# Optimization experiments

Hardware: AMD Instinct MI355X
Metric: run time of the kernel (lower is better)

## Reference

```python
import jax, jax.numpy as jnp
import numpy as np

EMBED = 384
HEADS = 12
DH = EMBED // HEADS  # 32, lucidrains default dim_heads = dim // heads
EPS = 1e-5


def _layernorm(t, g, b):
    mu = jnp.mean(t, axis=-1, keepdims=True)
    var = jnp.mean(jnp.square(t - mu), axis=-1, keepdims=True)
    return (t - mu) * jax.lax.rsqrt(var + EPS) * g + b


def _self_attn(t2, Wq, Wkv, Wo, bo):
    # t2: (N, T, D) -> multi-head self attention (lucidrains SelfAttention)
    N, T, D = t2.shape
    q = t2 @ Wq
    k, v = jnp.split(t2 @ Wkv, 2, axis=-1)
    def split_heads(z):
        return z.reshape(N, T, HEADS, DH).transpose(0, 2, 1, 3)  # (N,H,T,DH)
    q, k, v = map(split_heads, (q, k, v))
    dots = jnp.einsum('nhie,nhje->nhij', q, k) * (DH ** -0.5)
    o = jnp.einsum('nhij,nhje->nhie', jax.nn.softmax(dots, axis=-1), v)
    o = o.transpose(0, 2, 1, 3).reshape(N, T, D)
    return o @ Wo + bo


def _axial(xcl, axis, Wq, Wkv, Wo, bo):
    # xcl channels-last: (b, 3, 16, 16, C); attend along `axis` (1, 2 or 3)
    y = jnp.moveaxis(xcl, axis, -2)
    sh = y.shape
    o = _self_attn(y.reshape(-1, sh[-2], sh[-1]), Wq, Wkv, Wo, bo)
    return jnp.moveaxis(o.reshape(sh), -2, axis)


def setup_inputs() -> dict:
    key = jax.random.key(0)
    ks = jax.random.split(key, 24)
    d, mlp = EMBED, 4 * EMBED
    s = 0.02
    inp = {'x': jax.random.normal(ks[0], (128, 384, 3, 16, 16), jnp.float32)}
    for i in range(3):  # one SelfAttention per axial dim (slice, h, w)
        inp[f'Wq{i}'] = (jax.random.normal(ks[1 + 3 * i], (d, d)) * s).astype(jnp.float32)
        inp[f'Wkv{i}'] = (jax.random.normal(ks[2 + 3 * i], (d, 2 * d)) * s).astype(jnp.float32)
        inp[f'Wo{i}'] = (jax.random.normal(ks[3 + 3 * i], (d, d)) * s).astype(jnp.float32)
        inp[f'bo{i}'] = jnp.zeros((d,), jnp.float32)
    inp['g1'] = jnp.ones((d,), jnp.float32)
    inp['be1'] = jnp.zeros((d,), jnp.float32)
    inp['W1m'] = (jax.random.normal(ks[10], (d, mlp)) * s).astype(jnp.float32)
    inp['b1m'] = jnp.zeros((mlp,), jnp.float32)
    inp['W2m'] = (jax.random.normal(ks[11], (mlp, d)) * s).astype(jnp.float32)
    inp['b2m'] = jnp.zeros((d,), jnp.float32)
    inp['g2'] = jnp.ones((d,), jnp.float32)
    inp['be2'] = jnp.zeros((d,), jnp.float32)
    return inp


def reference(x, Wq0, Wkv0, Wo0, bo0, Wq1, Wkv1, Wo1, bo1, Wq2, Wkv2, Wo2, bo2,
              g1, be1, W1m, b1m, W2m, b2m, g2, be2):
    # x: (B, C=384, 3, 16, 16); dropout is identity in eval mode
    xcl = jnp.moveaxis(x, 1, -1)  # (B, 3, 16, 16, C)
    attn = (_axial(xcl, 1, Wq0, Wkv0, Wo0, bo0)
            + _axial(xcl, 2, Wq1, Wkv1, Wo1, bo1)
            + _axial(xcl, 3, Wq2, Wkv2, Wo2, bo2))  # sum_axial_out=True
    xcl = xcl + attn  # residual
    B = xcl.shape[0]
    t = xcl.reshape(B, 3 * 16 * 16, EMBED)  # == x.flatten(2).transpose(1,2)
    t = _layernorm(t, g1, be1)
    m = jax.nn.gelu(t @ W1m + b1m, approximate=False) @ W2m + b2m
    t = _layernorm(t + m, g2, be2)
    return jnp.moveaxis(t.reshape(B, 3, 16, 16, EMBED), -1, 1)
```

## Files before the change

kernel.cpp:

```cpp
#include <hip/hip_runtime.h>

typedef unsigned short u16;
typedef __bf16 bf16;
typedef bf16  bf16x4 __attribute__((ext_vector_type(4)));
typedef bf16  bf16x8 __attribute__((ext_vector_type(8)));
typedef float f32x4  __attribute__((ext_vector_type(4)));

__device__ __forceinline__ u16  f2b(float v) { return __builtin_bit_cast(u16, (bf16)v); }
__device__ __forceinline__ float b2f(u16 b)  { return (float)__builtin_bit_cast(bf16, b); }

__global__ void probe_dtype(const float* xf, int* flag) {
    __shared__ int cnt[256];
    const int tid = threadIdx.x;
    int good = 0;
#pragma unroll
    for (int i = 0; i < 4; ++i) {
        const float a = fabsf(xf[tid * 4 + i]);
        if (a > 9.5e-7f && a < 1.0e6f) good++;
    }
    cnt[tid] = good;
    __syncthreads();
    if (tid == 0) { int s = 0; for (int i = 0; i < 256; ++i) s += cnt[i]; *flag = (s > 512) ? 1 : 0; }
}

__global__ void cvt_vec(const void* in, bf16* out, int n, const int* flag) {
    const int f32 = *flag;
    for (int i = blockIdx.x * 256 + threadIdx.x; i < n; i += gridDim.x * 256)
        out[i] = f32 ? (bf16)(((const float*)in)[i])
                     : __builtin_bit_cast(bf16, ((const u16*)in)[i]);
}

__global__ void sum3_vec(const void* a, const void* b, const void* c, bf16* out, int n, const int* flag) {
    const int f32 = *flag;
    for (int i = blockIdx.x * 256 + threadIdx.x; i < n; i += gridDim.x * 256) {
        float va, vb, vc;
        if (f32) { va = ((const float*)a)[i]; vb = ((const float*)b)[i]; vc = ((const float*)c)[i]; }
        else { va = b2f(((const u16*)a)[i]); vb = b2f(((const u16*)b)[i]); vc = b2f(((const u16*)c)[i]); }
        out[i] = (bf16)(va + vb + vc);
    }
}

__global__ void transpose_cvt(const void* in, u16* out, size_t base_off, int R, int C, int ostride, const int* flag) {
    __shared__ u16 tile[32][34];
    const int f32 = *flag;
    const int c0 = blockIdx.x * 32, r0 = blockIdx.y * 32;
    const size_t bi = base_off + (size_t)blockIdx.z * R * C;
    const size_t bo = (size_t)blockIdx.z * C * ostride;
    const int tx = threadIdx.x, ty = threadIdx.y;
#pragma unroll
    for (int i = 0; i < 4; ++i) {
        const size_t idx = bi + (size_t)(r0 + ty + i * 8) * C + c0 + tx;
        tile[ty + i * 8][tx] = f32 ? f2b(((const float*)in)[idx]) : ((const u16*)in)[idx];
    }
    __syncthreads();
#pragma unroll
    for (int i = 0; i < 4; ++i)
        out[bo + (size_t)(c0 + ty + i * 8) * ostride + r0 + tx] = tile[tx][ty + i * 8];
}

__global__ void transpose_out(const u16* in, void* out, size_t base_off, int R, int C, const int* flag) {
    __shared__ u16 tile[32][34];
    const int f32 = *flag;
    const int c0 = blockIdx.x * 32, r0 = blockIdx.y * 32;
    const size_t bi = (size_t)blockIdx.z * R * C;
    const size_t bo = base_off + (size_t)blockIdx.z * R * C;
    const int tx = threadIdx.x, ty = threadIdx.y;
#pragma unroll
    for (int i = 0; i < 4; ++i)
        tile[ty + i * 8][tx] = in[bi + (size_t)(r0 + ty + i * 8) * C + c0 + tx];
    __syncthreads();
#pragma unroll
    for (int i = 0; i < 4; ++i) {
        const size_t o = bo + (size_t)(c0 + ty + i * 8) * R + r0 + tx;
        const u16 v = tile[tx][ty + i * 8];
        if (f32) ((float*)out)[o] = b2f(v); else ((u16*)out)[o] = v;
    }
}

__device__ __forceinline__ void gld_lds16(const bf16* g, bf16* l) {
    __builtin_amdgcn_global_load_lds((__attribute__((address_space(1))) void*)g,
                                     (__attribute__((address_space(3))) void*)l,
                                     16, 0, 0);
}

template<int MODE>
__global__ __launch_bounds__(512)
void gemm256(const bf16* __restrict__ A, const bf16* __restrict__ BT,
             bf16* C, const bf16* __restrict__ bias, int M, int N, int K)
{
    __shared__ __align__(16) bf16 sm[65536];
    const int tid = threadIdx.x;

    const int gx = gridDim.x, gy = gridDim.y;
    int lin = blockIdx.y * gx + blockIdx.x;
    const int nwg = gx * gy;
    const int q = nwg >> 3, r8 = nwg & 7;
    const int xcd = lin & 7, idx = lin >> 3;
    lin = (xcd < r8 ? xcd * (q + 1) : r8 * (q + 1) + (xcd - r8) * q) + idx;
    const int bm0 = (lin / gy) * 256;
    const int bn0 = (lin % gy) * 256;

    const int lane = tid & 63, wid = tid >> 6;
    const int wr = wid >> 2, wc = wid & 3;
    const int fr = lane & 15, fg = lane >> 4;
    const int arow = tid >> 3;
    const int scol = ((tid & 7) ^ (arow & 7)) << 3;

    const bf16* Ab = A  + (size_t)(bm0 + arow) * K + scol;
    const bf16* Bb = BT + (size_t)(bn0 + arow) * K + scol;

    bf16* const lA0 = sm;
    bf16* const lA1 = sm + 16384;
    bf16* const lB0 = sm + 32768;
    bf16* const lB1 = sm + 49152;

    f32x4 acc[8][4] = {};
    const int NT = K >> 6;

#pragma unroll
    for (int i = 0; i < 4; ++i) gld_lds16(Ab + (size_t)i * 64 * K, lA0 + i * 4096 + tid * 8);
#pragma unroll
    for (int i = 0; i < 4; ++i) gld_lds16(Bb + (size_t)i * 64 * K, lB0 + i * 4096 + tid * 8);
    __syncthreads();

    const int sw = fr & 7;
    for (int t = 0; t < NT; ++t) {
        if (t + 1 < NT) {
            const int k0 = (t + 1) << 6;
            bf16* la = ((t + 1) & 1) ? lA1 : lA0;
            bf16* lb = ((t + 1) & 1) ? lB1 : lB0;
#pragma unroll
            for (int i = 0; i < 4; ++i) gld_lds16(Ab + k0 + (size_t)i * 64 * K, la + i * 4096 + tid * 8);
#pragma unroll
            for (int i = 0; i < 4; ++i) gld_lds16(Bb + k0 + (size_t)i * 64 * K, lb + i * 4096 + tid * 8);
        }
        const bf16* la = (t & 1) ? lA1 : lA0;
        const bf16* lb = (t & 1) ? lB1 : lB0;
#pragma unroll
        for (int kk = 0; kk < 2; ++kk) {
            const int so = ((((kk << 2) + fg) ^ sw) << 3);
            bf16x8 bfv[4];
#pragma unroll
            for (int n = 0; n < 4; ++n)
                bfv[n] = *(const bf16x8*)&lb[(wc * 64 + n * 16 + fr) * 64 + so];
#pragma unroll
            for (int m = 0; m < 8; ++m) {
                const bf16x8 af = *(const bf16x8*)&la[(wr * 128 + m * 16 + fr) * 64 + so];
#pragma unroll
                for (int n = 0; n < 4; ++n)
                    acc[m][n] = __builtin_amdgcn_mfma_f32_16x16x32_bf16(af, bfv[n], acc[m][n], 0, 0, 0);
            }
        }
        __syncthreads();
    }

#pragma unroll
    for (int n = 0; n < 4; ++n) {
        const int col = wc * 64 + n * 16 + fr;
        const float bv = (MODE == 2) ? (float)bias[bn0 + col] : 0.f;
#pragma unroll
        for (int m = 0; m < 8; ++m) {
            const int row0 = wr * 128 + m * 16 + fg * 4;
#pragma unroll
            for (int r = 0; r < 4; ++r) {
                float v = acc[m][n][r];
                if (MODE == 2) { v += bv; v = 0.5f * v * (1.f + erff(v * 0.70710678118654752f)); }
                sm[(row0 + r) * 256 + col] = (bf16)v;
            }
        }
    }
    __syncthreads();
#pragma unroll
    for (int it = 0; it < 16; ++it) {
        const int chunk = it * 512 + tid;
        const int row = chunk >> 5, c8 = (chunk & 31) << 3;
        *(bf16x8*)&C[(size_t)(bm0 + row) * N + bn0 + c8] = *(const bf16x8*)&sm[row * 256 + c8];
    }
}

template<int MODE>
__global__ __launch_bounds__(256)
void gemm_bt(const bf16* __restrict__ A, const bf16* __restrict__ BT,
             bf16* C, const bf16* __restrict__ bias,
             const bf16* add, int M, int N, int K)
{
    __shared__ __align__(16) bf16 sm[16384];
    const int tid = threadIdx.x;

    const int gx = gridDim.x, gy = gridDim.y;
    int lin = blockIdx.y * gx + blockIdx.x;
    const int nwg = gx * gy;
    const int q = nwg >> 3, r8 = nwg & 7;
    const int xcd = lin & 7, idx = lin >> 3;
    lin = (xcd < r8 ? xcd * (q + 1) : r8 * (q + 1) + (xcd - r8) * q) + idx;
    const int bm0 = (lin / gy) * 128;
    const int bn0 = (lin % gy) * 128;

    const int lane = tid & 63, wid = tid >> 6;
    const int wr = wid >> 1, wc = wid & 1;
    const int fr = lane & 15, fg = lane >> 4;
    const int arow = tid >> 3;
    const int scol = ((tid & 7) ^ (arow & 7)) << 3;

    const bf16* Ab = A  + (size_t)(bm0 + arow) * K + scol;
    const bf16* Bb = BT + (size_t)(bn0 + arow) * K + scol;

    bf16* const lA = sm;
    bf16* const lB = sm + 8192;

    f32x4 acc[4][4] = {};
    const int NT = K >> 6;
    const int sw = fr & 7;

    for (int t = 0; t < NT; ++t) {
        __syncthreads();
        const int k0 = t << 6;
#pragma unroll
        for (int i = 0; i < 4; ++i) gld_lds16(Ab + k0 + (size_t)i * 32 * K, lA + i * 2048 + tid * 8);
#pragma unroll
        for (int i = 0; i < 4; ++i) gld_lds16(Bb + k0 + (size_t)i * 32 * K, lB + i * 2048 + tid * 8);
        __syncthreads();
#pragma unroll
        for (int kk = 0; kk < 2; ++kk) {
            bf16x8 af[4], bfv[4];
#pragma unroll
            for (int m = 0; m < 4; ++m)
                af[m] = *(const bf16x8*)&lA[(wr * 64 + m * 16 + fr) * 64 + ((((kk << 2) + fg) ^ sw) << 3)];
#pragma unroll
            for (int n = 0; n < 4; ++n)
                bfv[n] = *(const bf16x8*)&lB[(wc * 64 + n * 16 + fr) * 64 + ((((kk << 2) + fg) ^ sw) << 3)];
#pragma unroll
            for (int m = 0; m < 4; ++m)
#pragma unroll
                for (int n = 0; n < 4; ++n)
                    acc[m][n] = __builtin_amdgcn_mfma_f32_16x16x32_bf16(af[m], bfv[n], acc[m][n], 0, 0, 0);
        }
    }
    __syncthreads();

    float* lc = (float*)sm;
#pragma unroll
    for (int half = 0; half < 2; ++half) {
        if (wr == half) {
#pragma unroll
            for (int n = 0; n < 4; ++n) {
                const int col = wc * 64 + n * 16 + fr;
#pragma unroll
                for (int m = 0; m < 4; ++m)
#pragma unroll
                    for (int r2 = 0; r2 < 4; ++r2)
                        lc[(m * 16 + fg * 4 + r2) * 128 + col] = acc[m][n][r2];
            }
        }
        __syncthreads();
#pragma unroll
        for (int i = 0; i < 8; ++i) {
            const int chunk = i * 256 + tid;
            const int row = chunk >> 5, cb = (chunk & 31) * 4;
            const size_t goff = (size_t)(bm0 + half * 64 + row) * N + bn0 + cb;
            const f32x4 v = ((const f32x4*)lc)[chunk];
            bf16x4 o;
            if (MODE == 1) {
                const bf16x4 bv = *(const bf16x4*)&bias[bn0 + cb];
                const bf16x4 av = *(const bf16x4*)&add[goff];
#pragma unroll
                for (int e = 0; e < 4; ++e) o[e] = (bf16)(v[e] + (float)bv[e] + (float)av[e]);
            } else {
#pragma unroll
                for (int e = 0; e < 4; ++e) o[e] = (bf16)v[e];
            }
            *(bf16x4*)&C[goff] = o;
        }
        __syncthreads();
    }
}

__global__ __launch_bounds__(256)
void attn16(const bf16* __restrict__ QKV, bf16* __restrict__ O, int tstride, int lastmul, int qs, int os)
{
    const int lane = threadIdx.x & 63;
    const int gw   = (blockIdx.x * 256 + threadIdx.x) >> 6;
    const int head = gw % 12;
    const int seq  = gw / 12;
    const int b    = seq / 48, r2 = seq % 48;
    const int s    = r2 >> 4, last = r2 & 15;
    const int tbase = b * 768 + s * 256 + last * lastmul;
    const int fr = lane & 15, fg = lane >> 4;

    const size_t rowQ = (size_t)(tbase + fr * tstride) * qs + head * 32 + fg * 8;
    const bf16x8 kf = *(const bf16x8*)(QKV + rowQ + 384);
    const bf16x8 qf = *(const bf16x8*)(QKV + rowQ);
    const f32x4 z = {0.f, 0.f, 0.f, 0.f};
    f32x4 S = __builtin_amdgcn_mfma_f32_16x16x32_bf16(kf, qf, z, 0, 0, 0);

    const float sc = 0.17677669529663687f;
    float mx = fmaxf(fmaxf(S[0], S[1]), fmaxf(S[2], S[3]));
    mx = fmaxf(mx, __shfl_xor(mx, 16));
    mx = fmaxf(mx, __shfl_xor(mx, 32));
    float p[4], sum = 0.f;
#pragma unroll
    for (int r = 0; r < 4; ++r) { p[r] = __expf((S[r] - mx) * sc); sum += p[r]; }
    sum += __shfl_xor(sum, 16);
    sum += __shfl_xor(sum, 32);
    const float inv = 1.f / sum;

    bf16x8 pa;
#pragma unroll
    for (int j = 0; j < 8; ++j) {
        const int srcg = 2 * fg + (j >> 2);
        const float v = __shfl(p[j & 3], fr + 16 * (srcg & 3));
        pa[j] = (bf16)(fg < 2 ? v * inv : 0.f);
    }

#pragma unroll
    for (int t = 0; t < 2; ++t) {
        bf16x8 vf;
#pragma unroll
        for (int j = 0; j < 8; ++j) {
            const int key = fg * 8 + j;
            vf[j] = (fg < 2)
                ? QKV[(size_t)(tbase + key * tstride) * qs + 768 + head * 32 + fr + 16 * t]
                : (bf16)0.f;
        }
        f32x4 o = __builtin_amdgcn_mfma_f32_16x16x32_bf16(pa, vf, z, 0, 0, 0);
#pragma unroll
        for (int r = 0; r < 4; ++r)
            O[(size_t)(tbase + (fg * 4 + r) * tstride) * os + head * 32 + fr + 16 * t] = (bf16)o[r];
    }
}

__global__ __launch_bounds__(256)
void attn3(const bf16* __restrict__ QKV, bf16* __restrict__ O, int qs, int os)
{
    const int t    = blockIdx.x * 256 + threadIdx.x;
    const int head = t % 12;
    const int seq  = t / 12;
    const int b    = seq >> 8, hw = seq & 255;
    const size_t base  = (size_t)(b * 768 + hw) * qs + head * 32;
    const size_t tstep = (size_t)256 * qs;

    float s[3][3] = {};
#pragma unroll
    for (int c = 0; c < 4; ++c) {
        bf16x8 q[3], k[3];
#pragma unroll
        for (int i = 0; i < 3; ++i) {
            q[i] = *(const bf16x8*)(QKV + base + i * tstep + c * 8);
            k[i] = *(const bf16x8*)(QKV + base + i * tstep + 384 + c * 8);
        }
#pragma unroll
        for (int i = 0; i < 3; ++i)
#pragma unroll
            for (int j = 0; j < 3; ++j) {
                float a = 0.f;
#pragma unroll
                for (int e = 0; e < 8; ++e) a += (float)q[i][e] * (float)k[j][e];
                s[i][j] += a;
            }
    }
    const float sc = 0.17677669529663687f;
    float p[3][3];
#pragma unroll
    for (int i = 0; i < 3; ++i) {
        const float mx = fmaxf(s[i][0], fmaxf(s[i][1], s[i][2]));
        float sum = 0.f;
#pragma unroll
        for (int j = 0; j < 3; ++j) { p[i][j] = __expf((s[i][j] - mx) * sc); sum += p[i][j]; }
        const float inv = 1.f / sum;
#pragma unroll
        for (int j = 0; j < 3; ++j) p[i][j] *= inv;
    }
    const size_t obase = (size_t)(b * 768 + hw) * os + head * 32;
#pragma unroll
    for (int c = 0; c < 4; ++c) {
        bf16x8 v[3];
#pragma unroll
        for (int j = 0; j < 3; ++j) v[j] = *(const bf16x8*)(QKV + base + j * tstep + 768 + c * 8);
#pragma unroll
        for (int i = 0; i < 3; ++i) {
            bf16x8 ov;
#pragma unroll
            for (int e = 0; e < 8; ++e)
                ov[e] = (bf16)(p[i][0] * (float)v[0][e] + p[i][1] * (float)v[1][e] + p[i][2] * (float)v[2][e]);
            *(bf16x8*)(O + obase + (size_t)i * 256 * os + c * 8) = ov;
        }
    }
}

__global__ __launch_bounds__(256)
void ln_kernel(const bf16* __restrict__ in, bf16* __restrict__ out,
               const bf16* __restrict__ g, const bf16* __restrict__ be, int ntok)
{
    const int w    = (blockIdx.x * 256 + threadIdx.x) >> 6;
    const int lane = threadIdx.x & 63;
    if (w >= ntok) return;
    const bf16* row = in + (size_t)w * 384;
    float x[6], sum = 0.f;
#pragma unroll
    for (int i = 0; i < 6; ++i) { x[i] = (float)row[lane + i * 64]; sum += x[i]; }
#pragma unroll
    for (int o = 32; o >= 1; o >>= 1) sum += __shfl_xor(sum, o);
    const float mu = sum * (1.f / 384.f);
    float vs = 0.f;
#pragma unroll
    for (int i = 0; i < 6; ++i) { const float d = x[i] - mu; vs += d * d; }
#pragma unroll
    for (int o = 32; o >= 1; o >>= 1) vs += __shfl_xor(vs, o);
    const float rstd = rsqrtf(vs * (1.f / 384.f) + 1e-5f);
    bf16* orow = out + (size_t)w * 384;
#pragma unroll
    for (int i = 0; i < 6; ++i)
        orow[lane + i * 64] = (bf16)((x[i] - mu) * rstd * (float)g[lane + i * 64] + (float)be[lane + i * 64]);
}

extern "C" void kernel_launch(void* const* d_in, const int* in_sizes, int n_in,
                              void* d_out, int out_size, void* d_ws, size_t ws_size,
                              hipStream_t stream)
{
    const void* x = d_in[0];
    const void *Wq[3], *Wkv[3], *Wo[3], *bo[3];
    for (int i = 0; i < 3; ++i) {
        Wq[i]  = d_in[1 + 4 * i];
        Wkv[i] = d_in[2 + 4 * i];
        Wo[i]  = d_in[3 + 4 * i];
        bo[i]  = d_in[4 + 4 * i];
    }
    const void* g1  = d_in[13];
    const void* be1 = d_in[14];
    const void* W1m = d_in[15];
    const void* b1m = d_in[16];
    const void* W2m = d_in[17];
    const void* b2m = d_in[18];
    const void* g2  = d_in[19];
    const void* be2 = d_in[20];

    char* ws = (char*)d_ws;
    bf16* qkvT = (bf16*)(ws);
    bf16* woTf = (bf16*)(ws + 2654208ull);
    bf16* w1mT = (bf16*)(ws + 3538944ull);
    bf16* w2mT = (bf16*)(ws + 4718592ull);
    bf16 *vboS, *vg1, *vbe1, *vg2, *vbe2, *vb1m, *vb2m;
    {
        char* vp = ws + 5898240ull;
        vboS = (bf16*)(vp);
        vg1  = (bf16*)(vp + 768);        vbe1 = (bf16*)(vp + 1536);
        vg2  = (bf16*)(vp + 2304);       vbe2 = (bf16*)(vp + 3072);
        vb1m = (bf16*)(vp + 3840);       vb2m = (bf16*)(vp + 6912);
    }
    int* dflag = (int*)(ws + 5909504ull);
    const size_t WB = 6553600ull;

    int NB = 32;
    while (NB > 2) {
        size_t need = WB + (size_t)NB * 768 * (3 * 384 + 2 * 1152 + 1536) * 2;
        if (need <= ws_size) break;
        NB >>= 1;
    }
    const int Tc = NB * 768;
    const size_t tokB = (size_t)Tc * 384 * 2;
    bf16* Xc    = (bf16*)(ws + WB);
    bf16* ABc   = (bf16*)(ws + WB + tokB);
    bf16* T1c   = (bf16*)(ws + WB + 2 * tokB);
    bf16* ATOc  = (bf16*)(ws + WB + 3 * tokB);
    bf16* QKVc  = (bf16*)(ws + WB + 6 * tokB);
    bf16* BIGc  = (bf16*)(ws + WB + 9 * tokB);

    probe_dtype<<<1, 256, 0, stream>>>((const float*)x, dflag);
    sum3_vec<<<2, 256, 0, stream>>>(bo[0], bo[1], bo[2], vboS, 384, dflag);
    cvt_vec<<<2, 256, 0, stream>>>(g1,  vg1,  384,  dflag);
    cvt_vec<<<2, 256, 0, stream>>>(be1, vbe1, 384,  dflag);
    cvt_vec<<<2, 256, 0, stream>>>(g2,  vg2,  384,  dflag);
    cvt_vec<<<2, 256, 0, stream>>>(be2, vbe2, 384,  dflag);
    cvt_vec<<<6, 256, 0, stream>>>(b1m, vb1m, 1536, dflag);
    cvt_vec<<<2, 256, 0, stream>>>(b2m, vb2m, 384,  dflag);

    const dim3 tb(32, 8);
    for (int i = 0; i < 3; ++i) {
        transpose_cvt<<<dim3(12, 12, 1), tb, 0, stream>>>(Wq[i],  (u16*)(qkvT + (size_t)(i * 1152) * 384),       0, 384, 384, 384, dflag);
        transpose_cvt<<<dim3(24, 12, 1), tb, 0, stream>>>(Wkv[i], (u16*)(qkvT + (size_t)(i * 1152 + 384) * 384), 0, 384, 768, 384, dflag);
        transpose_cvt<<<dim3(12, 12, 1), tb, 0, stream>>>(Wo[i],  (u16*)(woTf + i * 384),                        0, 384, 384, 1152, dflag);
    }
    transpose_cvt<<<dim3(48, 12, 1), tb, 0, stream>>>(W1m, (u16*)w1mT, 0, 384, 1536, 384,  dflag);
    transpose_cvt<<<dim3(12, 48, 1), tb, 0, stream>>>(W2m, (u16*)w2mT, 0, 1536, 384, 1536, dflag);

    for (int b0 = 0; b0 < 128; b0 += NB) {
        const size_t xoff = (size_t)b0 * 384 * 768;
        transpose_cvt<<<dim3(24, 12, NB), tb, 0, stream>>>(x, (u16*)Xc, xoff, 384, 768, 384, dflag);

        for (int i = 0; i < 3; ++i) {
            gemm_bt<0><<<dim3(Tc / 128, 9), 256, 0, stream>>>(Xc, qkvT + (size_t)(i * 1152) * 384,
                                                              QKVc, nullptr, nullptr, Tc, 1152, 384);
            if (i == 0)      attn3 <<<NB * 12,  256, 0, stream>>>(QKVc, ATOc,              1152, 1152);
            else if (i == 1) attn16<<<NB * 144, 256, 0, stream>>>(QKVc, ATOc + 384, 16, 1, 1152, 1152);
            else             attn16<<<NB * 144, 256, 0, stream>>>(QKVc, ATOc + 768, 1, 16, 1152, 1152);
        }

        gemm_bt<1><<<dim3(Tc / 128, 3), 256, 0, stream>>>(ATOc, woTf, ABc, vboS, Xc, Tc, 384, 1152);

        ln_kernel<<<Tc / 4, 256, 0, stream>>>(ABc, T1c, vg1, vbe1, Tc);
        gemm256<2><<<dim3(Tc / 256, 6), 512, 0, stream>>>(T1c, w1mT, BIGc, vb1m, Tc, 1536, 384);
        gemm_bt<1><<<dim3(Tc / 128, 3), 256, 0, stream>>>(BIGc, w2mT, ABc, vb2m, T1c, Tc, 384, 1536);
        ln_kernel<<<Tc / 4, 256, 0, stream>>>(ABc, Xc, vg2, vbe2, Tc);
        transpose_out<<<dim3(12, 24, NB), tb, 0, stream>>>((const u16*)Xc, d_out, xoff, 768, 384, dflag);
    }
}
```

Measured before the change: 1.515 ms.

## Single-buffer gemm256 LDS and split epilogue into two halves

Cuts the gemm256 shared-memory footprint from 128KB to 64KB. The double-buffered prefetch of the next K-tile goes away: each iteration now loads into a single buffer and synchronises before computing. The epilogue stages and writes the 256x256 output tile in two 128-row halves so it fits the smaller buffer. The likely aim is to fit two workgroups per CU for occupancy, at the cost of losing the overlap between global loads and MFMA compute and adding extra barriers.

```diff
diff --git a/kernel.cpp b/kernel.cpp
--- a/kernel.cpp
+++ b/kernel.cpp
@@ -88,7 +88,7 @@
 void gemm256(const bf16* __restrict__ A, const bf16* __restrict__ BT,
              bf16* C, const bf16* __restrict__ bias, int M, int N, int K)
 {
-    __shared__ __align__(16) bf16 sm[65536];
+    __shared__ __align__(16) bf16 sm[32768];
     const int tid = threadIdx.x;
 
     const int gx = gridDim.x, gy = gridDim.y;
@@ -109,72 +109,67 @@
     const bf16* Ab = A  + (size_t)(bm0 + arow) * K + scol;
     const bf16* Bb = BT + (size_t)(bn0 + arow) * K + scol;
 
-    bf16* const lA0 = sm;
-    bf16* const lA1 = sm + 16384;
-    bf16* const lB0 = sm + 32768;
-    bf16* const lB1 = sm + 49152;
+    bf16* const lA = sm;
+    bf16* const lB = sm + 16384;
 
     f32x4 acc[8][4] = {};
     const int NT = K >> 6;
-
-#pragma unroll
-    for (int i = 0; i < 4; ++i) gld_lds16(Ab + (size_t)i * 64 * K, lA0 + i * 4096 + tid * 8);
-#pragma unroll
-    for (int i = 0; i < 4; ++i) gld_lds16(Bb + (size_t)i * 64 * K, lB0 + i * 4096 + tid * 8);
-    __syncthreads();
-
     const int sw = fr & 7;
+
     for (int t = 0; t < NT; ++t) {
-        if (t + 1 < NT) {
-            const int k0 = (t + 1) << 6;
-            bf16* la = ((t + 1) & 1) ? lA1 : lA0;
-            bf16* lb = ((t + 1) & 1) ? lB1 : lB0;
-#pragma unroll
-            for (int i = 0; i < 4; ++i) gld_lds16(Ab + k0 + (size_t)i * 64 * K, la + i * 4096 + tid * 8);
-#pragma unroll
-            for (int i = 0; i < 4; ++i) gld_lds16(Bb + k0 + (size_t)i * 64 * K, lb + i * 4096 + tid * 8);
-        }
-        const bf16* la = (t & 1) ? lA1 : lA0;
-        const bf16* lb = (t & 1) ? lB1 : lB0;
+        __syncthreads();
+        const int k0 = t << 6;
+#pragma unroll
+        for (int i = 0; i < 4; ++i) gld_lds16(Ab + k0 + (size_t)i * 64 * K, lA + i * 4096 + tid * 8);
+#pragma unroll
+        for (int i = 0; i < 4; ++i) gld_lds16(Bb + k0 + (size_t)i * 64 * K, lB + i * 4096 + tid * 8);
+        __syncthreads();
 #pragma unroll
         for (int kk = 0; kk < 2; ++kk) {
             const int so = ((((kk << 2) + fg) ^ sw) << 3);
             bf16x8 bfv[4];
 #pragma unroll
             for (int n = 0; n < 4; ++n)
-                bfv[n] = *(const bf16x8*)&lb[(wc * 64 + n * 16 + fr) * 64 + so];
+                bfv[n] = *(const bf16x8*)&lB[(wc * 64 + n * 16 + fr) * 64 + so];
 #pragma unroll
             for (int m = 0; m < 8; ++m) {
-                const bf16x8 af = *(const bf16x8*)&la[(wr * 128 + m * 16 + fr) * 64 + so];
+                const bf16x8 af = *(const bf16x8*)&lA[(wr * 128 + m * 16 + fr) * 64 + so];
 #pragma unroll
                 for (int n = 0; n < 4; ++n)
                     acc[m][n] = __builtin_amdgcn_mfma_f32_16x16x32_bf16(af, bfv[n], acc[m][n], 0, 0, 0);
             }
         }
-        __syncthreads();
-    }
-
-#pragma unroll
-    for (int n = 0; n < 4; ++n) {
-        const int col = wc * 64 + n * 16 + fr;
-        const float bv = (MODE == 2) ? (float)bias[bn0 + col] : 0.f;
-#pragma unroll
-        for (int m = 0; m < 8; ++m) {
-            const int row0 = wr * 128 + m * 16 + fg * 4;
-#pragma unroll
-            for (int r = 0; r < 4; ++r) {
-                float v = acc[m][n][r];
-                if (MODE == 2) { v += bv; v = 0.5f * v * (1.f + erff(v * 0.70710678118654752f)); }
-                sm[(row0 + r) * 256 + col] = (bf16)v;
+    }
+    __syncthreads();
+
+#pragma unroll
+    for (int half = 0; half < 2; ++half) {
+        if (wr == half) {
+#pragma unroll
+            for (int n = 0; n < 4; ++n) {
+                const int col = wc * 64 + n * 16 + fr;
+                const float bv = (MODE == 2) ? (float)bias[bn0 + col] : 0.f;
+#pragma unroll
+                for (int m = 0; m < 8; ++m) {
+                    const int row0 = m * 16 + fg * 4;
+#pragma unroll
+                    for (int r = 0; r < 4; ++r) {
+                        float v = acc[m][n][r];
+                        if (MODE == 2) { v += bv; v = 0.5f * v * (1.f + erff(v * 0.70710678118654752f)); }
+                        sm[(row0 + r) * 256 + col] = (bf16)v;
+                    }
+                }
             }
         }
-    }
-    __syncthreads();
-#pragma unroll
-    for (int it = 0; it < 16; ++it) {
-        const int chunk = it * 512 + tid;
-        const int row = chunk >> 5, c8 = (chunk & 31) << 3;
-        *(bf16x8*)&C[(size_t)(bm0 + row) * N + bn0 + c8] = *(const bf16x8*)&sm[row * 256 + c8];
+        __syncthreads();
+#pragma unroll
+        for (int it = 0; it < 8; ++it) {
+            const int chunk = it * 512 + tid;
+            const int row = chunk >> 5, c8 = (chunk & 31) << 3;
+            *(bf16x8*)&C[(size_t)(bm0 + half * 128 + row) * N + bn0 + c8]
+                = *(const bf16x8*)&sm[row * 256 + c8];
+        }
+        __syncthreads();
     }
 }
 
```

Result: slower. 1.731 ms (+14.2%).
